# Kernel tuning notes

Hardware: AMD Instinct MI355X
Metric: run time of the kernel (lower is better)

## Reference

```python
import jax, jax.numpy as jnp
import numpy as np

NSUM = 100   # number of Fourier-series terms in fupn
NPROD = 10   # number of sinc factors in the atomic characteristic function
N_ORDER = 1  # fupn order n


def _sinc(z):
    # unnormalized sinc: sin(z)/z  (jnp.sinc is normalized sin(pi z)/(pi z))
    return jnp.sinc(z / jnp.pi)


def fupn(z, n=N_ORDER, nsum=NSUM, nprod=NPROD):
    """Atomic basis function fup_n evaluated via its Fourier series.

    fup_n has compact support [-a, a] with a = (n+2)/2. Its Fourier transform
    is F_n(t) = sinc(t/2)^n * prod_{j=1}^{inf} sinc(t/2^j), truncated at nprod.
    fup_n(z) = (1/(2a)) * [1 + 2*sum_{k=1}^{nsum} F_n(pi k / a) cos(pi k z / a)].
    """
    a = (n + 2) / 2.0
    k = jnp.arange(1, nsum + 1, dtype=z.dtype)
    t = (jnp.pi / a) * k                      # (nsum,)
    c = _sinc(t / 2.0) ** n
    for j in range(1, nprod + 1):             # small fixed hyperparam loop
        c = c * _sinc(t / (2.0 ** j))
    # series: 0.5 + sum_k c_k cos(t_k z), contracted over the nsum axis
    phase = z[..., None] * t                  # (B, I, D, nsum)
    s = 0.5 + jnp.einsum('...k,k->...', jnp.cos(phase), c)
    return jnp.where(jnp.abs(z) <= a, s / a, jnp.zeros_like(s))


def setup_inputs() -> dict:
    key = jax.random.key(0)
    k1, k2 = jax.random.split(key)
    B, I, O, degree = 256, 128, 256, 32
    D = degree + 1
    x = jax.random.uniform(k1, (B, I), jnp.float32, minval=-1.0, maxval=1.0)
    # nn.init.normal_(std = 1/(input_dim*(degree+1)))
    atomic_coeffs = jax.random.normal(k2, (I, O, D), jnp.float32) * (1.0 / (I * D))
    centers = jnp.linspace(-1.0, 1.0, D).astype(jnp.float32)
    # compression = 1/center_spacing = degree / (range width) = 32/2 = 16
    compression = jnp.full((D,), degree / 2.0, dtype=jnp.float32)
    return {"x": x, "atomic_coeffs": atomic_coeffs,
            "compression": compression, "centers": centers}


def reference(x, atomic_coeffs, compression, centers):
    # x: (B, I) -> (B, I, 1); centers/compression: (D,) -> (1, 1, D)
    scaled_x = (x[:, :, None] - centers[None, None, :]) * compression[None, None, :]
    atomic_basis = fupn(scaled_x)                       # (B, I, D)
    y = jnp.einsum('bid,iod->bo', atomic_basis, atomic_coeffs)  # (B, O)
    return y
```

## Files before the change

### kernel.cpp

```cpp
#include <hip/hip_runtime.h>
#include <math.h>

#define B_    256
#define I_    128
#define O_    256
#define D_    33
#define NSUM  100
#define NPROD 10
#define A_SUP 1.5f
#define PI_F  3.14159265358979323846f

__global__ __launch_bounds__(256) void transpose_w(const float* __restrict__ W,
                                                   float* __restrict__ Wt) {
    const int i = blockIdx.x;
    __shared__ float ld[O_ * D_];
    const float* src = W + (size_t)i * O_ * D_;
    for (int t = threadIdx.x; t < O_ * D_; t += blockDim.x)
        ld[t] = src[t];
    __syncthreads();
    float* dst = Wt + (size_t)i * D_ * O_;
    for (int t = threadIdx.x; t < D_ * O_; t += blockDim.x) {
        const int d = t >> 8;
        const int o = t & (O_ - 1);
        dst[t] = ld[o * D_ + d];
    }
}

template <bool USE_WT>
__global__ __launch_bounds__(512, 2) void kan_main(const float* __restrict__ x,
                                                   const float* __restrict__ W,
                                                   const float* __restrict__ comp,
                                                   const float* __restrict__ cen,
                                                   float* __restrict__ y) {
    const int b   = blockIdx.x;
    const int tid = threadIdx.x;

    __shared__ float sc[NSUM];
    __shared__ float sx[I_];
    __shared__ int   sd0[I_];
    __shared__ float sbasis[I_][4];
    __shared__ float spart[512];

    if (tid < NSUM) {
        const float k = (float)(tid + 1);
        const float t = PI_F * k / A_SUP;
        float z0 = 0.5f * t;
        float c  = sinf(z0) / z0;
        float div = 0.5f;
        #pragma unroll
        for (int j = 1; j <= NPROD; ++j) {
            const float zz = t * div;
            c *= sinf(zz) / zz;
            div *= 0.5f;
        }
        sc[tid] = c;
    }

    if (tid < I_) {
        const float xv = x[b * I_ + tid];
        sx[tid] = xv;
        const float lo = 16.0f * (xv + 1.0f) - A_SUP;
        int d0 = (int)ceilf(lo);
        d0 = min(max(d0, 0), D_ - 4);
        sd0[tid] = d0;
    }
    __syncthreads();

    {
        const int i  = tid >> 2;
        const int dd = tid & 3;
        const int d  = sd0[i] + dd;
        const float z = (sx[i] - cen[d]) * comp[d];
        float s = 0.0f;
        if (fabsf(z) <= A_SUP) {
            const float th   = (PI_F / A_SUP) * z;
            const float c1   = cosf(th);
            float ckm1 = c1, ckm2 = 1.0f;
            s = 0.5f + sc[0] * c1;
            #pragma unroll 4
            for (int k = 2; k <= NSUM; ++k) {
                const float ck = 2.0f * c1 * ckm1 - ckm2;
                s += sc[k - 1] * ck;
                ckm2 = ckm1;
                ckm1 = ck;
            }
            s *= (1.0f / A_SUP);
        }
        sbasis[i][dd] = s;
    }
    __syncthreads();

    const int o = tid & (O_ - 1);
    const int h = tid >> 8;
    float acc = 0.0f;
    const int i_lo = h * (I_ / 2);
    if (USE_WT) {
        #pragma unroll 4
        for (int i = i_lo; i < i_lo + I_ / 2; ++i) {
            const int d0 = sd0[i];
            const float* wp = W + (((size_t)(i * D_ + d0)) << 8) + o;
            const float b0 = sbasis[i][0], b1 = sbasis[i][1];
            const float b2 = sbasis[i][2], b3 = sbasis[i][3];
            acc += b0 * wp[0]       + b1 * wp[O_]
                 + b2 * wp[2 * O_]  + b3 * wp[3 * O_];
        }
    } else {
        #pragma unroll 4
        for (int i = i_lo; i < i_lo + I_ / 2; ++i) {
            const int d0 = sd0[i];
            const float* wp = W + ((size_t)(i * O_ + o)) * D_ + d0;
            acc += sbasis[i][0] * wp[0] + sbasis[i][1] * wp[1]
                 + sbasis[i][2] * wp[2] + sbasis[i][3] * wp[3];
        }
    }
    spart[tid] = acc;
    __syncthreads();
    if (tid < O_)
        y[b * O_ + tid] = spart[tid] + spart[tid + O_];
}

extern "C" void kernel_launch(void* const* d_in, const int* in_sizes, int n_in,
                              void* d_out, int out_size, void* d_ws, size_t ws_size,
                              hipStream_t stream) {
    const float* x    = (const float*)d_in[0];
    const float* W    = (const float*)d_in[1];
    const float* comp = (const float*)d_in[2];
    const float* cen  = (const float*)d_in[3];
    float* y = (float*)d_out;

    const size_t wt_bytes = (size_t)I_ * D_ * O_ * sizeof(float);
    if (ws_size >= wt_bytes) {
        float* Wt = (float*)d_ws;
        transpose_w<<<I_, 256, 0, stream>>>(W, Wt);
        kan_main<true><<<B_, 512, 0, stream>>>(x, Wt, comp, cen, y);
    } else {
        kan_main<false><<<B_, 512, 0, stream>>>(x, W, comp, cen, y);
    }
}
```

Baseline: 86.10 us.

## Split input dimension across blocks and reduce with atomics

The main kernel now launches four blocks per batch row, each handling a 32-input chunk, and accumulates partial outputs into y with atomicAdd after zeroing y with a memset. The aim is more blocks in flight (1024 instead of 256) on the many-CU GPU and shorter per-block serial loops. In exchange it adds a memset, atomic traffic, and nondeterministic summation order. It also drops the fallback path for a small workspace, which assumes the workspace is always large enough.

```diff
diff --git a/kernel.cpp b/kernel.cpp
--- a/kernel.cpp
+++ b/kernel.cpp
@@ -9,6 +9,9 @@
 #define NPROD 10
 #define A_SUP 1.5f
 #define PI_F  3.14159265358979323846f
+
+#define ICHUNK 32
+#define NCHUNK (I_ / ICHUNK)
 
 __global__ __launch_bounds__(256) void transpose_w(const float* __restrict__ W,
                                                    float* __restrict__ Wt) {
@@ -26,19 +29,20 @@
     }
 }
 
-template <bool USE_WT>
-__global__ __launch_bounds__(512, 2) void kan_main(const float* __restrict__ x,
-                                                   const float* __restrict__ W,
+__global__ __launch_bounds__(512, 4) void kan_main(const float* __restrict__ x,
+                                                   const float* __restrict__ Wt,
                                                    const float* __restrict__ comp,
                                                    const float* __restrict__ cen,
                                                    float* __restrict__ y) {
-    const int b   = blockIdx.x;
-    const int tid = threadIdx.x;
+    const int b     = blockIdx.x >> 2;
+    const int chunk = blockIdx.x & (NCHUNK - 1);
+    const int i0    = chunk * ICHUNK;
+    const int tid   = threadIdx.x;
 
     __shared__ float sc[NSUM];
-    __shared__ float sx[I_];
-    __shared__ int   sd0[I_];
-    __shared__ float sbasis[I_][4];
+    __shared__ float sx[ICHUNK];
+    __shared__ int   sd0[ICHUNK];
+    __shared__ float sbasis[ICHUNK][4];
     __shared__ float spart[512];
 
     if (tid < NSUM) {
@@ -56,8 +60,8 @@
         sc[tid] = c;
     }
 
-    if (tid < I_) {
-        const float xv = x[b * I_ + tid];
+    if (tid < ICHUNK) {
+        const float xv = x[b * I_ + i0 + tid];
         sx[tid] = xv;
         const float lo = 16.0f * (xv + 1.0f) - A_SUP;
         int d0 = (int)ceilf(lo);
@@ -66,7 +70,7 @@
     }
     __syncthreads();
 
-    {
+    if (tid < ICHUNK * 4) {
         const int i  = tid >> 2;
         const int dd = tid & 3;
         const int d  = sd0[i] + dd;
@@ -93,30 +97,20 @@
     const int o = tid & (O_ - 1);
     const int h = tid >> 8;
     float acc = 0.0f;
-    const int i_lo = h * (I_ / 2);
-    if (USE_WT) {
-        #pragma unroll 4
-        for (int i = i_lo; i < i_lo + I_ / 2; ++i) {
-            const int d0 = sd0[i];
-            const float* wp = W + (((size_t)(i * D_ + d0)) << 8) + o;
-            const float b0 = sbasis[i][0], b1 = sbasis[i][1];
-            const float b2 = sbasis[i][2], b3 = sbasis[i][3];
-            acc += b0 * wp[0]       + b1 * wp[O_]
-                 + b2 * wp[2 * O_]  + b3 * wp[3 * O_];
-        }
-    } else {
-        #pragma unroll 4
-        for (int i = i_lo; i < i_lo + I_ / 2; ++i) {
-            const int d0 = sd0[i];
-            const float* wp = W + ((size_t)(i * O_ + o)) * D_ + d0;
-            acc += sbasis[i][0] * wp[0] + sbasis[i][1] * wp[1]
-                 + sbasis[i][2] * wp[2] + sbasis[i][3] * wp[3];
-        }
+    const int i_lo = h * (ICHUNK / 2);
+    #pragma unroll 4
+    for (int il = i_lo; il < i_lo + ICHUNK / 2; ++il) {
+        const int d0 = sd0[il];
+        const float* wp = Wt + ((((size_t)(i0 + il)) * D_ + d0) << 8) + o;
+        const float b0 = sbasis[il][0], b1 = sbasis[il][1];
+        const float b2 = sbasis[il][2], b3 = sbasis[il][3];
+        acc += b0 * wp[0]      + b1 * wp[O_]
+             + b2 * wp[2 * O_] + b3 * wp[3 * O_];
     }
     spart[tid] = acc;
     __syncthreads();
     if (tid < O_)
-        y[b * O_ + tid] = spart[tid] + spart[tid + O_];
+        atomicAdd(&y[b * O_ + tid], spart[tid] + spart[tid + O_]);
 }
 
 extern "C" void kernel_launch(void* const* d_in, const int* in_sizes, int n_in,
@@ -128,12 +122,9 @@
     const float* cen  = (const float*)d_in[3];
     float* y = (float*)d_out;
 
-    const size_t wt_bytes = (size_t)I_ * D_ * O_ * sizeof(float);
-    if (ws_size >= wt_bytes) {
-        float* Wt = (float*)d_ws;
-        transpose_w<<<I_, 256, 0, stream>>>(W, Wt);
-        kan_main<true><<<B_, 512, 0, stream>>>(x, Wt, comp, cen, y);
-    } else {
-        kan_main<false><<<B_, 512, 0, stream>>>(x, W, comp, cen, y);
-    }
+    float* Wt = (float*)d_ws;
+
+    hipMemsetAsync(y, 0, (size_t)out_size * sizeof(float), stream);
+    transpose_w<<<I_, 256, 0, stream>>>(W, Wt);
+    kan_main<<<B_ * NCHUNK, 512, 0, stream>>>(x, Wt, comp, cen, y);
 }
```

Measured after the change: 86.95 us. About the same (+1.0%).

## Store transposed weights as bf16 and precompute series coefficients once

Applied to the files above, without the earlier changes.

The transpose kernel now writes the weight tensor in bf16 instead of fp32, halving the workspace traffic for both the write and the gather in the main kernel. It also computes the 100 Fourier coefficients once into the workspace rather than in every block. The main kernel reads bf16 pairs per thread, with each thread handling two outputs and four input slices, and reduces across four partial sums. Weight precision drops to bf16, which may affect accuracy, and the fallback path for a small workspace is removed.

```diff
diff --git a/kernel.cpp b/kernel.cpp
--- a/kernel.cpp
+++ b/kernel.cpp
@@ -1,4 +1,5 @@
 #include <hip/hip_runtime.h>
+#include <hip/hip_bf16.h>
 #include <math.h>
 
 #define B_    256
@@ -10,39 +11,18 @@
 #define A_SUP 1.5f
 #define PI_F  3.14159265358979323846f
 
+#define WT_ELEMS ((size_t)I_ * D_ * O_)
+
 __global__ __launch_bounds__(256) void transpose_w(const float* __restrict__ W,
-                                                   float* __restrict__ Wt) {
+                                                   __hip_bfloat16* __restrict__ Wt,
+                                                   float* __restrict__ scW) {
     const int i = blockIdx.x;
     __shared__ float ld[O_ * D_];
     const float* src = W + (size_t)i * O_ * D_;
     for (int t = threadIdx.x; t < O_ * D_; t += blockDim.x)
         ld[t] = src[t];
-    __syncthreads();
-    float* dst = Wt + (size_t)i * D_ * O_;
-    for (int t = threadIdx.x; t < D_ * O_; t += blockDim.x) {
-        const int d = t >> 8;
-        const int o = t & (O_ - 1);
-        dst[t] = ld[o * D_ + d];
-    }
-}
-
-template <bool USE_WT>
-__global__ __launch_bounds__(512, 2) void kan_main(const float* __restrict__ x,
-                                                   const float* __restrict__ W,
-                                                   const float* __restrict__ comp,
-                                                   const float* __restrict__ cen,
-                                                   float* __restrict__ y) {
-    const int b   = blockIdx.x;
-    const int tid = threadIdx.x;
-
-    __shared__ float sc[NSUM];
-    __shared__ float sx[I_];
-    __shared__ int   sd0[I_];
-    __shared__ float sbasis[I_][4];
-    __shared__ float spart[512];
-
-    if (tid < NSUM) {
-        const float k = (float)(tid + 1);
+    if (i == 0 && threadIdx.x < NSUM) {
+        const float k = (float)(threadIdx.x + 1);
         const float t = PI_F * k / A_SUP;
         float z0 = 0.5f * t;
         float c  = sinf(z0) / z0;
@@ -53,8 +33,31 @@
             c *= sinf(zz) / zz;
             div *= 0.5f;
         }
-        sc[tid] = c;
+        scW[threadIdx.x] = c;
     }
+    __syncthreads();
+    __hip_bfloat16* dst = Wt + (size_t)i * D_ * O_;
+    for (int t = threadIdx.x; t < D_ * O_; t += blockDim.x) {
+        const int d = t >> 8;
+        const int o = t & (O_ - 1);
+        dst[t] = __float2bfloat16(ld[o * D_ + d]);
+    }
+}
+
+__global__ __launch_bounds__(512, 2) void kan_main(const float* __restrict__ x,
+                                                   const __hip_bfloat16* __restrict__ Wt,
+                                                   const float* __restrict__ comp,
+                                                   const float* __restrict__ cen,
+                                                   const float* __restrict__ scW,
+                                                   float* __restrict__ y) {
+    const int b   = blockIdx.x;
+    const int tid = threadIdx.x;
+
+    __shared__ float sc[NSUM];
+    __shared__ float sx[I_];
+    __shared__ int   sd0[I_];
+    __shared__ float sbasis[I_][4];
+    __shared__ float spart[4][O_];
 
     if (tid < I_) {
         const float xv = x[b * I_ + tid];
@@ -64,6 +67,8 @@
         d0 = min(max(d0, 0), D_ - 4);
         sd0[tid] = d0;
     }
+    if (tid >= 384 && tid < 384 + NSUM)
+        sc[tid - 384] = scW[tid - 384];
     __syncthreads();
 
     {
@@ -73,8 +78,8 @@
         const float z = (sx[i] - cen[d]) * comp[d];
         float s = 0.0f;
         if (fabsf(z) <= A_SUP) {
-            const float th   = (PI_F / A_SUP) * z;
-            const float c1   = cosf(th);
+            const float th = (PI_F / A_SUP) * z;
+            const float c1 = cosf(th);
             float ckm1 = c1, ckm2 = 1.0f;
             s = 0.5f + sc[0] * c1;
             #pragma unroll 4
@@ -90,33 +95,37 @@
     }
     __syncthreads();
 
-    const int o = tid & (O_ - 1);
-    const int h = tid >> 8;
-    float acc = 0.0f;
-    const int i_lo = h * (I_ / 2);
-    if (USE_WT) {
-        #pragma unroll 4
-        for (int i = i_lo; i < i_lo + I_ / 2; ++i) {
-            const int d0 = sd0[i];
-            const float* wp = W + (((size_t)(i * D_ + d0)) << 8) + o;
-            const float b0 = sbasis[i][0], b1 = sbasis[i][1];
-            const float b2 = sbasis[i][2], b3 = sbasis[i][3];
-            acc += b0 * wp[0]       + b1 * wp[O_]
-                 + b2 * wp[2 * O_]  + b3 * wp[3 * O_];
-        }
-    } else {
-        #pragma unroll 4
-        for (int i = i_lo; i < i_lo + I_ / 2; ++i) {
-            const int d0 = sd0[i];
-            const float* wp = W + ((size_t)(i * O_ + o)) * D_ + d0;
-            acc += sbasis[i][0] * wp[0] + sbasis[i][1] * wp[1]
-                 + sbasis[i][2] * wp[2] + sbasis[i][3] * wp[3];
-        }
+    const int p = tid & 127;
+    const int h = tid >> 7;
+    float acc0 = 0.0f, acc1 = 0.0f;
+    const int i_lo = h * 32;
+    #pragma unroll 4
+    for (int i = i_lo; i < i_lo + 32; ++i) {
+        const int d0 = sd0[i];
+        const ushort2* wp = (const ushort2*)
+            (Wt + ((((size_t)i) * D_ + d0) << 8)) + p;
+        const float b0 = sbasis[i][0], b1 = sbasis[i][1];
+        const float b2 = sbasis[i][2], b3 = sbasis[i][3];
+        const ushort2 w0 = wp[0];
+        const ushort2 w1 = wp[O_ / 2];
+        const ushort2 w2 = wp[O_];
+        const ushort2 w3 = wp[3 * (O_ / 2)];
+        acc0 += b0 * __bfloat162float(*(const __hip_bfloat16*)&w0.x)
+              + b1 * __bfloat162float(*(const __hip_bfloat16*)&w1.x)
+              + b2 * __bfloat162float(*(const __hip_bfloat16*)&w2.x)
+              + b3 * __bfloat162float(*(const __hip_bfloat16*)&w3.x);
+        acc1 += b0 * __bfloat162float(*(const __hip_bfloat16*)&w0.y)
+              + b1 * __bfloat162float(*(const __hip_bfloat16*)&w1.y)
+              + b2 * __bfloat162float(*(const __hip_bfloat16*)&w2.y)
+              + b3 * __bfloat162float(*(const __hip_bfloat16*)&w3.y);
     }
-    spart[tid] = acc;
+    spart[h][2 * p]     = acc0;
+    spart[h][2 * p + 1] = acc1;
     __syncthreads();
+
     if (tid < O_)
-        y[b * O_ + tid] = spart[tid] + spart[tid + O_];
+        y[b * O_ + tid] = spart[0][tid] + spart[1][tid]
+                        + spart[2][tid] + spart[3][tid];
 }
 
 extern "C" void kernel_launch(void* const* d_in, const int* in_sizes, int n_in,
@@ -128,12 +137,9 @@
     const float* cen  = (const float*)d_in[3];
     float* y = (float*)d_out;
 
-    const size_t wt_bytes = (size_t)I_ * D_ * O_ * sizeof(float);
-    if (ws_size >= wt_bytes) {
-        float* Wt = (float*)d_ws;
-        transpose_w<<<I_, 256, 0, stream>>>(W, Wt);
-        kan_main<true><<<B_, 512, 0, stream>>>(x, Wt, comp, cen, y);
-    } else {
-        kan_main<false><<<B_, 512, 0, stream>>>(x, W, comp, cen, y);
-    }
+    __hip_bfloat16* Wt = (__hip_bfloat16*)d_ws;
+    float* scW = (float*)((char*)d_ws + WT_ELEMS * sizeof(__hip_bfloat16));
+
+    transpose_w<<<I_, 256, 0, stream>>>(W, Wt, scW);
+    kan_main<<<B_, 512, 0, stream>>>(x, Wt, comp, cen, scW, y);
 }
```

New measurement: 82.51 us. 4.2% less time.
